# Kernel tuning notes

Measured on AMD Instinct MI355X. Metric: run time of the kernel, lower is better.

## Reference

```python
import jax, jax.numpy as jnp
import numpy as np

BATCH, IN_F, OUT_F = 1024, 512, 512
GRID_SIZE, SPLINE_ORDER = 32, 3
P_DEACTIVATE = 0.1


def b_splines(x, grid, k):
    """x: (n, in), grid: (in, G+2k+1) -> bases (n, in, G+k). Cox-de Boor recursion."""
    x = x[..., None]  # (n, in, 1)
    bases = ((x >= grid[:, :-1]) & (x < grid[:, 1:])).astype(x.dtype)
    for j in range(1, k + 1):
        left = (x - grid[:, : -(j + 1)]) / (grid[:, j:-1] - grid[:, : -(j + 1)])
        right = (grid[:, j + 1:] - x) / (grid[:, j + 1:] - grid[:, 1:-j])
        bases = left * bases[..., :-1] + right * bases[..., 1:]
    return bases


def setup_inputs() -> dict:
    key = jax.random.key(0)
    k1, k2, k3, k4, k5 = jax.random.split(key, 5)
    # uniform extended grid over [-1, 1], same for every input feature
    h = 2.0 / GRID_SIZE
    knots = np.arange(-SPLINE_ORDER, GRID_SIZE + SPLINE_ORDER + 1, dtype=np.float32) * h - 1.0
    grid = jnp.asarray(np.tile(knots, (IN_F, 1)))  # (in, G+2k+1)
    return {
        "x": jax.random.normal(k1, (BATCH, IN_F), jnp.float32),
        "base_weight": jax.random.normal(k2, (OUT_F, IN_F), jnp.float32) * 0.05,
        "spline_weight": jax.random.normal(k3, (OUT_F, IN_F, GRID_SIZE + SPLINE_ORDER), jnp.float32) * 0.1,
        "spline_scaler": jax.random.normal(k4, (OUT_F, IN_F), jnp.float32),
        "grid": grid,
        "deactivate_mask": jax.random.bernoulli(k5, P_DEACTIVATE, (OUT_F, IN_F)),
    }


def reference(x, base_weight, spline_weight, spline_scaler, grid, deactivate_mask):
    k = SPLINE_ORDER
    weights = spline_weight * spline_scaler[..., None]  # scaled_spline_weight (o, i, c)
    # base path: F.linear(silu(x), base_weight)
    base_out = jax.nn.silu(x) @ base_weight.T  # (b, o)
    # spline path
    bases = b_splines(x, grid, k)  # (b, i, c)
    contrib = jnp.einsum('bic,oic->boi', bases, weights)  # (b, o, i)
    # linear fallback from spline values at grid endpoints
    gmin = grid[:, k].min()
    gmax = grid[:, -k - 1].max()
    ends_x = jnp.stack([gmin, gmax])[:, None] * jnp.ones((1, x.shape[1]), x.dtype)  # (2, i)
    y_ends = jnp.einsum('nic,oic->noi', b_splines(ends_x, grid, k), weights)  # (2, o, i)
    y_start, y_end = y_ends[0], y_ends[1]
    dx = gmax - gmin
    degenerate = jnp.abs(dx) < 1e-8
    a = jnp.where(degenerate, 0.0, (y_end - y_start) / jnp.where(degenerate, 1.0, dx))  # (o, i)
    b = y_start - a * gmin
    lin = a[None] * x[:, None, :] + b[None]  # (b, o, i)
    final = jnp.where(deactivate_mask[None], lin, contrib)
    return base_out + final.sum(axis=2)
```

## Files before the change

### kernel.cpp

```cpp
#include <hip/hip_runtime.h>
#include <hip/hip_bf16.h>


typedef unsigned short u16;
typedef unsigned int u32;
typedef unsigned long long u64;
typedef __attribute__((ext_vector_type(8))) short short8;
typedef __attribute__((ext_vector_type(4))) float floatx4;
typedef __attribute__((ext_vector_type(4))) unsigned int uintx4;

#define IN_F 512
#define OUT_F 512
#define BATCH 1024
#define K_SPLINE (IN_F * 36)
#define K_BASE_OFF K_SPLINE
#define K_LIN_OFF (K_SPLINE + IN_F)
#define K_TOT (K_SPLINE + 2 * IN_F)
#define SPLITS 32
#define MN (BATCH * OUT_F)

static __device__ inline u16 f2b(float f) {
  union { float f; u32 u; } v; v.f = f;
  u32 r = v.u + 0x7FFFu + ((v.u >> 16) & 1u);
  return (u16)(r >> 16);
}
static __device__ inline float b2f(u32 lo16) {
  union { u32 u; float f; } v; v.u = lo16 << 16; return v.f;
}

__global__ __launch_bounds__(256) void prep_kernel(
    const float* __restrict__ bw, const float* __restrict__ sw,
    const float* __restrict__ sc, const void* __restrict__ maskp,
    const float* __restrict__ x, u16* __restrict__ B,
    float* __restrict__ bias_part, u64* __restrict__ PB8) {
  __shared__ u64 lds64[1120 * 4];
  __shared__ int sflag;
  __shared__ float ws4[4];
  int blk = blockIdx.x, t = threadIdx.x;

  if (blk >= 1024) {
    int id = (blk - 1024) * 256 + t;
    float xv = x[id];
    int mc = (int)floorf((xv + 1.1875f) * 16.0f);
    float gm = (float)mc * 0.0625f - 1.1875f;
    if (xv < gm) { mc -= 1; gm -= 0.0625f; }
    else if (xv >= gm + 0.0625f) { mc += 1; gm += 0.0625f; }
    u32 lo, hi;
    if (mc >= 0 && mc <= 37) {
      float t_ = (xv - gm) * 16.0f;
      float t2 = t_ * t_, t3 = t2 * t_;
      float omt = 1.0f - t_;
      u16 r0 = f2b(omt * omt * omt * (1.0f / 6.0f));
      u16 r1 = f2b((3.0f * t3 - 6.0f * t2 + 4.0f) * (1.0f / 6.0f));
      u16 r2 = f2b((-3.0f * t3 + 3.0f * t2 + 3.0f * t_ + 1.0f) * (1.0f / 6.0f));
      lo = (u32)r0 | ((u32)r1 << 16);
      hi = (u32)r2 | ((u32)mc << 16);
    } else {
      lo = 0; hi = 0xFFFF0000u;
    }
    PB8[id] = (u64)lo | ((u64)hi << 32);
    return;
  }

  float* lds_f = (float*)lds64;
  u16* lds_u = (u16*)lds64;
  int id = blk * 256 + t;
  int o = id >> 9, i = id & 511;
  int i0 = (blk & 1) * 256;

  const float* swb = sw + ((size_t)o * 512 + i0) * 35;
#pragma unroll
  for (int j = 0; j < 35; ++j) lds_f[j * 256 + t] = swb[j * 256 + t];

  const u32* mw = (const u32*)maskp;
  if (t == 0) sflag = 0;
  __syncthreads();
  if (t < 64) {
    u32 w2 = mw[blk * 64 + t];
    if ((w2 & 0xFFFFFF00u) && w2 != 0x3F800000u) atomicOr(&sflag, 1);
  }
  __syncthreads();
  int fl = sflag;
  if (!(fl & 1)) {
    u32 w1 = mw[blk * 256 + t];
    if (w1 == 0x3F800000u) atomicOr(&sflag, 2);
  }
  __syncthreads();
  fl = sflag;
  bool mk;
  if (fl & 1)      mk = ((const unsigned char*)maskp)[id] != 0;
  else if (fl & 2) mk = ((const float*)maskp)[id] != 0.0f;
  else             mk = ((const int*)maskp)[id] != 0;

  float s = sc[id];
  float w[35];
#pragma unroll
  for (int c = 0; c < 35; ++c) w[c] = lds_f[t * 35 + c] * s;
  __syncthreads();

  float ys = (w[0] + 4.0f * w[1] + w[2]) * (1.0f / 6.0f);
  float ye = (w[32] + 4.0f * w[33] + w[34]) * (1.0f / 6.0f);
  float a = (ye - ys) * 0.5f;
  float bl = ys + a;

#pragma unroll
  for (int c = 0; c < 35; ++c) lds_u[t * 36 + c] = f2b(mk ? 0.0f : w[c]);
  lds_u[t * 36 + 35] = 0;

  B[(size_t)o * K_TOT + K_BASE_OFF + i] = f2b(bw[id]);
  B[(size_t)o * K_TOT + K_LIN_OFF + i] = f2b(mk ? a : 0.0f);

  float v = mk ? bl : 0.0f;
#pragma unroll
  for (int off = 32; off >= 1; off >>= 1) v += __shfl_down(v, off);
  if ((t & 63) == 0) ws4[t >> 6] = v;
  __syncthreads();
  if (t == 0) bias_part[blk] = ws4[0] + ws4[1] + ws4[2] + ws4[3];

  u64* dst = (u64*)(B + (size_t)o * K_TOT + (size_t)i0 * 36);
#pragma unroll
  for (int j = 0; j < 9; ++j) dst[j * 256 + t] = lds64[j * 256 + t];
}

__global__ __launch_bounds__(256, 4) void gemm_fused(const float* __restrict__ x,
                                                     const u64* __restrict__ PB8,
                                                     const u16* __restrict__ Bp,
                                                     u16* __restrict__ P) {
  __shared__ u16 As[128 * 64 + 64];
  __shared__ u16 Bs[128 * 64];

  int t = threadIdx.x;
  int id = blockIdx.x;
  int ks = id >> 5, tile = id & 31;
  int bm = tile >> 2, bn = tile & 3;
  int w = t >> 6, l = t & 63;
  int wm = w & 1, wn = w >> 1;

  floatx4 acc[4][4];
#pragma unroll
  for (int p = 0; p < 4; ++p)
#pragma unroll
    for (int q = 0; q < 4; ++q) acc[p][q] = (floatx4)0.0f;

  int nit = (ks < 16) ? 10 : 9;
  int k0s = (ks < 16) ? ks * 640 : 10240 + (ks - 16) * 576;

  int ra = t >> 3;
  int cg = (t & 7) ^ (ra & 7);
  const u16* Bg = Bp + (size_t)(bn * 128 + ra) * K_TOT + k0s + cg * 8;
  u16* Bsp = Bs + t * 8;

  int rr_ = t >> 1, hf = t & 1;
  int rx7 = rr_ & 7;
  int dummy = 128 * 64 + (t & 63);
  const u64* PBrow = PB8 + (size_t)(bm * 128 + rr_) * IN_F;

  int mr = l & 15;
  int cq = l >> 4;

  int if_cur = 0; u64 e0 = 0, e1 = 0;
  if (k0s < K_BASE_OFF) {
    if_cur = (k0s + hf * 32) / 36;
    e0 = PBrow[if_cur];
    e1 = PBrow[if_cur + 1];
  }

  int k0 = k0s;
  for (int kk = 0; kk < nit; ++kk, k0 += 64) {
#pragma unroll
    for (int p = 0; p < 4; ++p)
      __builtin_amdgcn_global_load_lds(
          (const __attribute__((address_space(1))) void*)(Bg + (size_t)p * 32 * K_TOT),
          (__attribute__((address_space(3))) void*)(Bsp + p * 2048), 16, 0, 0);
    Bg += 64;

    int if_nxt = if_cur; u64 en0 = e0, en1 = e1;
    if (k0 < K_BASE_OFF) {
#pragma unroll
      for (int q = 0; q < 4; ++q) {
        int ch = hf * 4 + q;
        *(uintx4*)&As[rr_ * 64 + ((ch ^ rx7) << 3)] = (uintx4)0u;
      }
      int k0w = k0 + hf * 32;
      int i_last = (k0w + 31) / 36;
#pragma unroll
      for (int ii = 0; ii < 2; ++ii) {
        int i = if_cur + ii;
        if (i <= i_last) {
          u64 e = ii ? e1 : e0;
          u32 lo = (u32)e, hi = (u32)(e >> 32);
          int mc = (int)(hi >> 16);
          float f0 = b2f(lo & 0xFFFFu);
          float f1 = b2f(lo >> 16);
          float f2 = b2f(hi & 0xFFFFu);
          u16 bv[4] = {(u16)lo, (u16)(lo >> 16), (u16)hi, f2b(1.0f - f0 - f1 - f2)};
          int cb = i * 36 + mc - 3 - k0;
#pragma unroll
          for (int j = 0; j < 4; ++j) {
            int c = cb + j;
            bool ok = ((u32)(c - hf * 32) < 32u) && ((u32)(mc - 3 + j) < 35u);
            int addr = ok ? (rr_ * 64 + (((c >> 3) ^ rx7) << 3) + (c & 7)) : dummy;
            As[addr] = bv[j];
          }
        }
      }
      int k0n = k0 + 64;
      if (k0n < K_BASE_OFF) {
        if_nxt = (k0n + hf * 32) / 36;
        en0 = PBrow[if_nxt];
        en1 = PBrow[if_nxt + 1];
      }
    } else {
      bool isBase = (k0 < K_LIN_OFF);
      int xb = isBase ? (k0 - K_BASE_OFF) : (k0 - K_LIN_OFF);
#pragma unroll
      for (int p = 0; p < 4; ++p) {
        int cid = t + 256 * p;
        int row = cid >> 3, ch = cid & 7;
        const float* xp = &x[(size_t)(bm * 128 + row) * IN_F + xb + ch * 8];
        floatx4 v0 = *(const floatx4*)xp;
        floatx4 v1 = *(const floatx4*)(xp + 4);
        float f[8] = {v0.x, v0.y, v0.z, v0.w, v1.x, v1.y, v1.z, v1.w};
        u16 r[8];
#pragma unroll
        for (int j = 0; j < 8; ++j) {
          float vv = f[j];
          if (isBase) vv = vv / (1.0f + __expf(-vv));
          r[j] = f2b(vv);
        }
        *(short8*)(As + row * 64 + ((ch ^ (row & 7)) << 3)) = *(short8*)r;
      }
    }
    __syncthreads();

#pragma unroll
    for (int h = 0; h < 2; ++h) {
      short8 af[4], bf[4];
      int c = h * 4 + cq;
#pragma unroll
      for (int tm = 0; tm < 4; ++tm) {
        int row = wm * 64 + tm * 16 + mr;
        af[tm] = *(const short8*)&As[row * 64 + ((c ^ (row & 7)) << 3)];
      }
#pragma unroll
      for (int tn = 0; tn < 4; ++tn) {
        int row = wn * 64 + tn * 16 + mr;
        bf[tn] = *(const short8*)&Bs[row * 64 + ((c ^ (row & 7)) << 3)];
      }
#pragma unroll
      for (int tm = 0; tm < 4; ++tm)
#pragma unroll
        for (int tn = 0; tn < 4; ++tn)
          acc[tm][tn] = __builtin_amdgcn_mfma_f32_16x16x32_bf16(af[tm], bf[tn], acc[tm][tn], 0, 0, 0);
    }
    __syncthreads();
    if_cur = if_nxt; e0 = en0; e1 = en1;
  }

  u16* Pb = P + ((size_t)tile * SPLITS + ks) * 16384;
#pragma unroll
  for (int q = 0; q < 8; ++q) {
    int tm = q >> 1, tn0 = (q & 1) * 2;
    u16 r[8];
#pragma unroll
    for (int z = 0; z < 4; ++z) r[z] = f2b(acc[tm][tn0][z]);
#pragma unroll
    for (int z = 0; z < 4; ++z) r[4 + z] = f2b(acc[tm][tn0 + 1][z]);
    *(short8*)(Pb + q * 2048 + t * 8) = *(short8*)r;
  }
}

__global__ __launch_bounds__(256) void reduce_kernel(const u16* __restrict__ P,
                                                     const float* __restrict__ bias_part,
                                                     float* __restrict__ out) {
  int rid = blockIdx.x * 256 + threadIdx.x;
  int tile = rid >> 11;
  int rem = rid & 2047;
  int q = rem >> 8, t = rem & 255;
  const u16* base = P + (size_t)tile * SPLITS * 16384 + q * 2048 + t * 8;

  float s[8] = {0, 0, 0, 0, 0, 0, 0, 0};
#pragma unroll
  for (int ks = 0; ks < SPLITS; ++ks) {
    short8 v = *(const short8*)(base + (size_t)ks * 16384);
#pragma unroll
    for (int j = 0; j < 8; ++j) s[j] += b2f((u32)(u16)v[j]);
  }

  int w = t >> 6, l = t & 63;
  int wm = w & 1, wn = w >> 1;
  int bm = tile >> 2, bn = tile & 3;
  int row0 = bm * 128 + wm * 64 + ((l >> 4) << 2);
  int col0 = bn * 128 + wn * 64 + (l & 15);
  int tm = q >> 1, tn0 = (q & 1) * 2;
#pragma unroll
  for (int j = 0; j < 8; ++j) {
    int tn = tn0 + (j >> 2), rr = j & 3;
    int row = row0 + tm * 16 + rr;
    int col = col0 + tn * 16;
    float bsv = bias_part[2 * col] + bias_part[2 * col + 1];
    out[(size_t)row * OUT_F + col] = s[j] + bsv;
  }
}

extern "C" void kernel_launch(void* const* d_in, const int* in_sizes, int n_in,
                              void* d_out, int out_size, void* d_ws, size_t ws_size,
                              hipStream_t stream) {
  const float* x  = (const float*)d_in[0];
  const float* bw = (const float*)d_in[1];
  const float* sw = (const float*)d_in[2];
  const float* sc = (const float*)d_in[3];
  const void* mask = d_in[5];

  const size_t B_BYTES = (size_t)OUT_F * K_TOT * 2;
  const size_t BIAS_OFF = B_BYTES;
  const size_t PB_OFF = B_BYTES + 8192;
  const size_t PB_BYTES = (size_t)MN * 8;
  const size_t P_OFF = PB_OFF + PB_BYTES;

  char* wsb = (char*)d_ws;
  u16* Bpack = (u16*)wsb;
  float* bias_part = (float*)(wsb + BIAS_OFF);
  u64* PB8 = (u64*)(wsb + PB_OFF);
  u16* P = (u16*)(wsb + P_OFF);

  prep_kernel<<<3072, 256, 0, stream>>>(bw, sw, sc, mask, x, Bpack, bias_part, PB8);
  gemm_fused<<<1024, 256, 0, stream>>>(x, PB8, Bpack, P);
  reduce_kernel<<<256, 256, 0, stream>>>(P, bias_part, (float*)d_out);
}
```

Baseline: 137.8 us.

## Double-buffer A tile in LDS and load B fragments directly into registers

Moves the B operand out of LDS: each wave now loads its MFMA B fragments straight from global memory into registers. A is double-buffered across two LDS buffers so the next tile is built while MFMAs consume the current one, which leaves one barrier per iteration instead of two. The occupancy hint is dropped from launch bounds. This trades more register pressure and uncoalesced, redundant B global loads (each wave reads its own rows) for overlap of the A build with compute and fewer barriers.

Measured after the change: 161.0 us. 16.8% more time.

```diff
diff --git a/kernel.cpp b/kernel.cpp
--- a/kernel.cpp
+++ b/kernel.cpp
@@ -18,6 +18,8 @@
 #define K_TOT (K_SPLINE + 2 * IN_F)
 #define SPLITS 32
 #define MN (BATCH * OUT_F)
+
+#define BARRIER_LGKM() asm volatile("s_waitcnt lgkmcnt(0)\n\ts_barrier" ::: "memory")
 
 static __device__ inline u16 f2b(float f) {
   union { float f; u32 u; } v; v.f = f;
@@ -122,12 +124,12 @@
   for (int j = 0; j < 9; ++j) dst[j * 256 + t] = lds64[j * 256 + t];
 }
 
-__global__ __launch_bounds__(256, 4) void gemm_fused(const float* __restrict__ x,
-                                                     const u64* __restrict__ PB8,
-                                                     const u16* __restrict__ Bp,
-                                                     u16* __restrict__ P) {
-  __shared__ u16 As[128 * 64 + 64];
-  __shared__ u16 Bs[128 * 64];
+__global__ __launch_bounds__(256) void gemm_fused(const float* __restrict__ x,
+                                                  const u64* __restrict__ PB8,
+                                                  const u16* __restrict__ Bp,
+                                                  u16* __restrict__ P) {
+  __shared__ u16 As0[128 * 64 + 64];
+  __shared__ u16 As1[128 * 64 + 64];
 
   int t = threadIdx.x;
   int id = blockIdx.x;
@@ -135,6 +137,7 @@
   int bm = tile >> 2, bn = tile & 3;
   int w = t >> 6, l = t & 63;
   int wm = w & 1, wn = w >> 1;
+  int mr = l & 15, cq = l >> 4;
 
   floatx4 acc[4][4];
 #pragma unroll
@@ -145,43 +148,33 @@
   int nit = (ks < 16) ? 10 : 9;
   int k0s = (ks < 16) ? ks * 640 : 10240 + (ks - 16) * 576;
 
-  int ra = t >> 3;
-  int cg = (t & 7) ^ (ra & 7);
-  const u16* Bg = Bp + (size_t)(bn * 128 + ra) * K_TOT + k0s + cg * 8;
-  u16* Bsp = Bs + t * 8;
+  const u16* Bgf = Bp + (size_t)(bn * 128 + wn * 64 + mr) * K_TOT + cq * 8;
 
   int rr_ = t >> 1, hf = t & 1;
   int rx7 = rr_ & 7;
-  int dummy = 128 * 64 + (t & 63);
   const u64* PBrow = PB8 + (size_t)(bm * 128 + rr_) * IN_F;
 
-  int mr = l & 15;
-  int cq = l >> 4;
-
   int if_cur = 0; u64 e0 = 0, e1 = 0;
-  if (k0s < K_BASE_OFF) {
-    if_cur = (k0s + hf * 32) / 36;
-    e0 = PBrow[if_cur];
-    e1 = PBrow[if_cur + 1];
-  }
-
-  int k0 = k0s;
-  for (int kk = 0; kk < nit; ++kk, k0 += 64) {
-#pragma unroll
-    for (int p = 0; p < 4; ++p)
-      __builtin_amdgcn_global_load_lds(
-          (const __attribute__((address_space(1))) void*)(Bg + (size_t)p * 32 * K_TOT),
-          (__attribute__((address_space(3))) void*)(Bsp + p * 2048), 16, 0, 0);
-    Bg += 64;
-
-    int if_nxt = if_cur; u64 en0 = e0, en1 = e1;
-    if (k0 < K_BASE_OFF) {
+
+  auto loadB = [&](short8 (&dst)[8], int k0b) {
+#pragma unroll
+    for (int h = 0; h < 2; ++h)
+#pragma unroll
+      for (int tn = 0; tn < 4; ++tn)
+        dst[h * 4 + tn] =
+            *(const short8*)(Bgf + (size_t)(tn * 16) * K_TOT + k0b + h * 32);
+  };
+
+  auto buildA = [&](int kkb, u16* A) {
+    int dummy = 128 * 64 + (t & 63);
+    int k0b = k0s + kkb * 64;
+    if (k0b < K_BASE_OFF) {
 #pragma unroll
       for (int q = 0; q < 4; ++q) {
         int ch = hf * 4 + q;
-        *(uintx4*)&As[rr_ * 64 + ((ch ^ rx7) << 3)] = (uintx4)0u;
-      }
-      int k0w = k0 + hf * 32;
+        *(uintx4*)&A[rr_ * 64 + ((ch ^ rx7) << 3)] = (uintx4)0u;
+      }
+      int k0w = k0b + hf * 32;
       int i_last = (k0w + 31) / 36;
 #pragma unroll
       for (int ii = 0; ii < 2; ++ii) {
@@ -194,25 +187,26 @@
           float f1 = b2f(lo >> 16);
           float f2 = b2f(hi & 0xFFFFu);
           u16 bv[4] = {(u16)lo, (u16)(lo >> 16), (u16)hi, f2b(1.0f - f0 - f1 - f2)};
-          int cb = i * 36 + mc - 3 - k0;
+          int cb = i * 36 + mc - 3 - k0b;
 #pragma unroll
           for (int j = 0; j < 4; ++j) {
             int c = cb + j;
             bool ok = ((u32)(c - hf * 32) < 32u) && ((u32)(mc - 3 + j) < 35u);
             int addr = ok ? (rr_ * 64 + (((c >> 3) ^ rx7) << 3) + (c & 7)) : dummy;
-            As[addr] = bv[j];
+            A[addr] = bv[j];
           }
         }
       }
-      int k0n = k0 + 64;
+      int k0n = k0b + 64;
       if (k0n < K_BASE_OFF) {
-        if_nxt = (k0n + hf * 32) / 36;
-        en0 = PBrow[if_nxt];
-        en1 = PBrow[if_nxt + 1];
+        int if_n = (k0n + hf * 32) / 36;
+        if_cur = if_n;
+        e0 = PBrow[if_n];
+        e1 = PBrow[if_n + 1];
       }
     } else {
-      bool isBase = (k0 < K_LIN_OFF);
-      int xb = isBase ? (k0 - K_BASE_OFF) : (k0 - K_LIN_OFF);
+      bool isBase = (k0b < K_LIN_OFF);
+      int xb = isBase ? (k0b - K_BASE_OFF) : (k0b - K_LIN_OFF);
 #pragma unroll
       for (int p = 0; p < 4; ++p) {
         int cid = t + 256 * p;
@@ -228,33 +222,52 @@
           if (isBase) vv = vv / (1.0f + __expf(-vv));
           r[j] = f2b(vv);
         }
-        *(short8*)(As + row * 64 + ((ch ^ (row & 7)) << 3)) = *(short8*)r;
+        *(short8*)(A + row * 64 + ((ch ^ (row & 7)) << 3)) = *(short8*)r;
       }
     }
-    __syncthreads();
-
+  };
+
+  auto mfmaStep = [&](const u16* A, short8 (&bf)[8]) {
 #pragma unroll
     for (int h = 0; h < 2; ++h) {
-      short8 af[4], bf[4];
+      short8 af[4];
       int c = h * 4 + cq;
 #pragma unroll
       for (int tm = 0; tm < 4; ++tm) {
         int row = wm * 64 + tm * 16 + mr;
-        af[tm] = *(const short8*)&As[row * 64 + ((c ^ (row & 7)) << 3)];
-      }
-#pragma unroll
-      for (int tn = 0; tn < 4; ++tn) {
-        int row = wn * 64 + tn * 16 + mr;
-        bf[tn] = *(const short8*)&Bs[row * 64 + ((c ^ (row & 7)) << 3)];
+        af[tm] = *(const short8*)&A[row * 64 + ((c ^ (row & 7)) << 3)];
       }
 #pragma unroll
       for (int tm = 0; tm < 4; ++tm)
 #pragma unroll
         for (int tn = 0; tn < 4; ++tn)
-          acc[tm][tn] = __builtin_amdgcn_mfma_f32_16x16x32_bf16(af[tm], bf[tn], acc[tm][tn], 0, 0, 0);
+          acc[tm][tn] = __builtin_amdgcn_mfma_f32_16x16x32_bf16(
+              af[tm], bf[h * 4 + tn], acc[tm][tn], 0, 0, 0);
     }
-    __syncthreads();
-    if_cur = if_nxt; e0 = en0; e1 = en1;
+  };
+
+  short8 bA[8], bB[8];
+
+  if (k0s < K_BASE_OFF) {
+    if_cur = (k0s + hf * 32) / 36;
+    e0 = PBrow[if_cur];
+    e1 = PBrow[if_cur + 1];
+  }
+  loadB(bA, k0s);
+  buildA(0, As0);
+  BARRIER_LGKM();
+
+  int k0 = k0s;
+  for (int kk = 0; kk < nit; kk += 2) {
+    if (kk + 1 < nit) { loadB(bB, k0 + 64); buildA(kk + 1, As1); }
+    mfmaStep(As0, bA);
+    BARRIER_LGKM();
+    k0 += 64;
+    if (kk + 1 >= nit) break;
+    if (kk + 2 < nit) { loadB(bA, k0 + 64); buildA(kk + 2, As0); }
+    mfmaStep(As1, bB);
+    BARRIER_LGKM();
+    k0 += 64;
   }
 
   u16* Pb = P + ((size_t)tile * SPLITS + ks) * 16384;
```
